# Kernel tuning notes

Measured on AMD Instinct MI355X. Metric: run time of the kernel, lower is better.

Reference implementation:

```python
import jax, jax.numpy as jnp
import numpy as np

EPS = 1e-5
NUM_HEADS = 16

def rmsnorm(x, w=None, eps=EPS):
    y = x * jax.lax.rsqrt(jnp.mean(x * x, axis=-1, keepdims=True) + eps)
    return y if w is None else y * w

def act_quant(x):
    # per-token 8-bit absmax activation quantization (BitNet b1.58)
    scale = 127.0 / jnp.clip(jnp.max(jnp.abs(x), axis=-1, keepdims=True), 1e-5, None)
    return jnp.clip(jnp.round(x * scale), -128, 127) / scale

def weight_quant(w):
    # ternary (1.58-bit) absmean weight quantization
    scale = 1.0 / jnp.clip(jnp.mean(jnp.abs(w)), 1e-5, None)
    return jnp.clip(jnp.round(w * scale), -1, 1) / scale

def bit_linear(x, w):
    # BitLinear: RMSNorm -> STE-quantized activation @ STE-quantized ternary weight
    xn = rmsnorm(x)
    xq = xn + jax.lax.stop_gradient(act_quant(xn) - xn)
    wq = w + jax.lax.stop_gradient(weight_quant(w) - w)
    return xq @ wq.T

def hgrn_recurrence(i, logf):
    # elementwise gated linear recurrence: h_t = exp(logf_t) * h_{t-1} + i_t
    def step(h, xs):
        ii, ff = xs
        h = jnp.exp(ff) * h + ii
        return h, h
    B, T, D = i.shape
    _, o = jax.lax.scan(step, jnp.zeros((B, D), i.dtype),
                        (jnp.swapaxes(i, 0, 1), jnp.swapaxes(logf, 0, 1)))
    return jnp.swapaxes(o, 0, 1)  # [B, T, D]

def hgrn_bit_attention(x, w_i, w_f, w_g, w_o, g_norm_w):
    i = bit_linear(x, w_i)
    f = bit_linear(x, w_f)
    logf = jax.nn.log_sigmoid(f)
    i = jax.nn.silu(i) * (1.0 - jax.nn.sigmoid(f))  # swiglu(i, 1 - sigmoid(f))
    o = hgrn_recurrence(i, logf)
    g = bit_linear(x, w_g)
    B, T, D = o.shape
    oh = rmsnorm(o.reshape(B, T, NUM_HEADS, D // NUM_HEADS), g_norm_w)  # per-head RMSNorm
    o = oh.reshape(B, T, D) * g * jax.nn.sigmoid(g)  # swish gate (FusedRMSNormSwishGate)
    return bit_linear(o, w_o)

def setup_inputs() -> dict:
    key = jax.random.key(0)
    B, S_S, S_C, D = 4, 4096, 512, 2048
    ks = jax.random.split(key, 16)
    mk = lambda k: jax.random.normal(k, (D, D), jnp.float32) * 0.02
    return {
        "hidden_states": jax.random.normal(ks[0], (B, S_S, D), jnp.float32),
        "encoder_hidden_states": jax.random.normal(ks[1], (B, S_C, D), jnp.float32),
        "w_q": mk(ks[2]), "w_k": mk(ks[3]), "w_v": mk(ks[4]), "w_out": mk(ks[5]),
        "w_add_q": mk(ks[6]), "w_add_k": mk(ks[7]), "w_add_v": mk(ks[8]), "w_add_out": mk(ks[9]),
        "w_i": mk(ks[10]), "w_f": mk(ks[11]), "w_g": mk(ks[12]), "w_o": mk(ks[13]),
        "g_norm_w": jnp.ones((D // NUM_HEADS,), jnp.float32),
    }

def reference(hidden_states, encoder_hidden_states, w_q, w_k, w_v, w_out,
              w_add_q, w_add_k, w_add_v, w_add_out, w_i, w_f, w_g, w_o, g_norm_w):
    q_s = bit_linear(hidden_states, w_q)
    k_s = bit_linear(hidden_states, w_k)          # computed as in original; unused by attn
    v_s = bit_linear(hidden_states, w_v)          # computed as in original; unused by attn
    q_c = bit_linear(encoder_hidden_states, w_add_q)
    k_c = bit_linear(encoder_hidden_states, w_add_k)
    v_c = bit_linear(encoder_hidden_states, w_add_v)
    q_joint = jnp.concatenate([q_c, q_s], axis=1)  # context first, then stream
    attn_out = hgrn_bit_attention(q_joint, w_i, w_f, w_g, w_o, g_norm_w)
    len_c = encoder_hidden_states.shape[1]
    out_c, out_s = attn_out[:, :len_c, :], attn_out[:, len_c:, :]
    return (bit_linear(out_s, w_out), bit_linear(out_c, w_add_out))
```

## Files before the change

kernel.cpp:

```cpp
#include <hip/hip_runtime.h>
#include <math.h>
#include <stdint.h>

#define D2 2048

typedef int v4i __attribute__((ext_vector_type(4)));
typedef int v16i __attribute__((ext_vector_type(16)));

struct Ptrs8 { const float* p[8]; };
struct RowMap { int seg, jump, off; };

enum { QW_Q = 0, QW_OUT = 1, QW_ADDQ = 2, QW_ADDOUT = 3, QW_I = 4, QW_F = 5, QW_G = 6, QW_O = 7 };

__device__ __forceinline__ int rmap(RowMap m, int r) {
  return (r / m.seg) * m.jump + (r % m.seg) + m.off;
}

__device__ __forceinline__ void gload16(const void* g, void* l) {
  __builtin_amdgcn_global_load_lds((__attribute__((address_space(1))) void*)g,
                                   (__attribute__((address_space(3))) void*)l, 16, 0, 0);
}

__device__ __forceinline__ float fsig(float x) {
  return __builtin_amdgcn_rcpf(1.0f + __expf(-x));
}

template <bool NT>
__device__ __forceinline__ void stf(float* p, float v) {
  if (NT) __builtin_nontemporal_store(v, p);
  else *p = v;
}

__device__ __forceinline__ void gswz(int nM, int& mb, int& nb) {
  int bid = blockIdx.x;
  int wg = (bid & 7) * (nM << 1) + (bid >> 3);
  mb = wg >> 4;
  nb = wg & 15;
}

__global__ __launch_bounds__(256) void k_wabs(Ptrs8 wsrc, double* part) {
  int m = blockIdx.y;
  const float4* w4 = (const float4*)(wsrc.p[m] + (size_t)blockIdx.x * 4096 + threadIdx.x * 16);
  double s = 0.0;
#pragma unroll
  for (int j = 0; j < 4; ++j) {
    float4 v = w4[j];
    s += (double)fabsf(v.x) + (double)fabsf(v.y) + (double)fabsf(v.z) + (double)fabsf(v.w);
  }
#pragma unroll
  for (int o = 32; o; o >>= 1) s += __shfl_down(s, o);
  __shared__ double red[4];
  if ((threadIdx.x & 63) == 0) red[threadIdx.x >> 6] = s;
  __syncthreads();
  if (threadIdx.x == 0) part[(size_t)m * 1024 + blockIdx.x] = red[0] + red[1] + red[2] + red[3];
}

__global__ __launch_bounds__(256) void k_wmean(const double* part, double* wqs, float* wmul) {
  int m = blockIdx.x, t = threadIdx.x;
  const double* p = part + (size_t)m * 1024;
  double s = p[t] + p[t + 256] + p[t + 512] + p[t + 768];
#pragma unroll
  for (int o = 32; o; o >>= 1) s += __shfl_down(s, o);
  __shared__ double red[4];
  if ((t & 63) == 0) red[t >> 6] = s;
  __syncthreads();
  if (t == 0) {
    double mean = (red[0] + red[1] + red[2] + red[3]) * (1.0 / 4194304.0);
    double cl = mean > 1e-5 ? mean : 1e-5;
    wqs[m] = 1.0 / cl;
    wmul[m] = (float)cl;
  }
}

__global__ __launch_bounds__(256) void k_wquant(Ptrs8 wsrc, const double* wqs, int8_t* wq) {
  int m = blockIdx.y;
  double qs = wqs[m];
  size_t base = (size_t)blockIdx.x * 4096 + threadIdx.x * 16;
  const float4* w4 = (const float4*)(wsrc.p[m] + base);
  union { int8_t b[16]; int4 v; } u;
#pragma unroll
  for (int j = 0; j < 4; ++j) {
    float4 v = w4[j];
    float f[4] = {v.x, v.y, v.z, v.w};
#pragma unroll
    for (int c = 0; c < 4; ++c) {
      int q = (int)rint((double)f[c] * qs);
      q = q > 1 ? 1 : (q < -1 ? -1 : q);
      u.b[j * 4 + c] = (int8_t)q;
    }
  }
  *(int4*)(wq + (size_t)m * 4194304 + base) = u.v;
}

__global__ __launch_bounds__(256) void k_actq(const float* __restrict__ x, int8_t* __restrict__ q,
                                              float* __restrict__ inv) {
  int row = blockIdx.x, t = threadIdx.x;
  const float4* xr = (const float4*)(x + (size_t)row * D2);
  float4 a = xr[t * 2], b = xr[t * 2 + 1];
  float v[8] = {a.x, a.y, a.z, a.w, b.x, b.y, b.z, b.w};
  float ss = 0.f, ma = 0.f;
#pragma unroll
  for (int j = 0; j < 8; ++j) { ss += v[j] * v[j]; ma = fmaxf(ma, fabsf(v[j])); }
#pragma unroll
  for (int o = 32; o; o >>= 1) { ss += __shfl_down(ss, o); ma = fmaxf(ma, __shfl_down(ma, o)); }
  __shared__ float rs[4], rm[4], bc[2];
  if ((t & 63) == 0) { rs[t >> 6] = ss; rm[t >> 6] = ma; }
  __syncthreads();
  if (t == 0) {
    float S = rs[0] + rs[1] + rs[2] + rs[3];
    float M = fmaxf(fmaxf(rm[0], rm[1]), fmaxf(rm[2], rm[3]));
    float r = 1.0f / sqrtf(S * (1.0f / 2048.0f) + 1e-5f);
    float mx = fmaxf(M * r, 1e-5f);
    bc[0] = r;
    bc[1] = 127.0f / mx;
    inv[row] = mx * (1.0f / 127.0f);
  }
  __syncthreads();
  float r = bc[0], s = bc[1];
  union { int8_t b8[8]; int2 p2; } u;
#pragma unroll
  for (int j = 0; j < 8; ++j) {
    float xn = v[j] * r;
    int qq = (int)rintf(xn * s);
    qq = qq > 127 ? 127 : (qq < -128 ? -128 : qq);
    u.b8[j] = (int8_t)qq;
  }
  ((int2*)(q + (size_t)row * D2))[t] = u.p2;
}

#define SYNC_PIPE(N)                                          \
  do {                                                        \
    __builtin_amdgcn_sched_barrier(0);                        \
    asm volatile("s_waitcnt vmcnt(" #N ")" ::: "memory");     \
    __builtin_amdgcn_sched_barrier(0);                        \
    __builtin_amdgcn_s_barrier();                             \
    __builtin_amdgcn_sched_barrier(0);                        \
  } while (0)

__device__ __forceinline__ void gemm_mainloop128(const int8_t* __restrict__ Aq,
                                                 const int8_t* __restrict__ Wq, int ga0, int ga1,
                                                 int n0, int t, int8_t* lds, v16i acc[2][2]) {
  const int wid = t >> 6, lane = t & 63;
  const int wr = wid >> 1, wc = wid & 1, am = lane & 31, g = lane >> 5;
  const int arow = t >> 2;
  const int achk = ((t & 3) ^ ((arow >> 1) & 3)) * 16;
  const int8_t* agp0 = Aq + (size_t)ga0 * 2048 + achk;
  const int8_t* agp1 = Aq + (size_t)ga1 * 2048 + achk;
  const int8_t* bgp0 = Wq + (size_t)(n0 + arow) * 2048 + achk;
  const int8_t* bgp1 = Wq + (size_t)(n0 + 64 + arow) * 2048 + achk;
  int8_t* A0 = lds;
  int8_t* B0 = lds + 8192;
  int8_t* A1 = lds + 16384;
  int8_t* B1 = lds + 24576;
  int8_t* A2 = lds + 32768;
  int8_t* B2 = lds + 40960;

#define STAGE128(Ab, Bb)                              \
  do {                                                \
    gload16(agp0, (Ab) + wid * 1024);                 \
    gload16(agp1, (Ab) + 4096 + wid * 1024);          \
    gload16(bgp0, (Bb) + wid * 1024);                 \
    gload16(bgp1, (Bb) + 4096 + wid * 1024);          \
    agp0 += 64; agp1 += 64; bgp0 += 64; bgp1 += 64;   \
  } while (0)

#define COMPUTE128(Ab, Bb)                                                                  \
  do {                                                                                      \
    _Pragma("unroll") for (int kk = 0; kk < 2; ++kk) {                                      \
      v4i af[2], bf[2];                                                                     \
      _Pragma("unroll") for (int mi = 0; mi < 2; ++mi) {                                    \
        int r = wr * 64 + mi * 32 + am;                                                     \
        int slot = ((kk << 1) | g) ^ ((r >> 1) & 3);                                        \
        af[mi] = *(const v4i*)((Ab) + r * 64 + slot * 16);                                  \
        int rb = wc * 64 + mi * 32 + am;                                                    \
        int slotb = ((kk << 1) | g) ^ ((rb >> 1) & 3);                                      \
        bf[mi] = *(const v4i*)((Bb) + rb * 64 + slotb * 16);                                \
      }                                                                                     \
      _Pragma("unroll") for (int mi = 0; mi < 2; ++mi)                                      \
        _Pragma("unroll") for (int ni = 0; ni < 2; ++ni)                                    \
          acc[mi][ni] =                                                                     \
              __builtin_amdgcn_mfma_i32_32x32x32_i8(af[mi], bf[ni], acc[mi][ni], 0, 0, 0);  \
    }                                                                                       \
  } while (0)

  STAGE128(A0, B0);
  STAGE128(A1, B1);
  STAGE128(A2, B2);
  SYNC_PIPE(8);
#pragma unroll 1
  for (int tt = 0; tt < 30; tt += 3) {
    COMPUTE128(A0, B0);
    SYNC_PIPE(4);
    if (tt + 3 < 32) STAGE128(A0, B0);
    COMPUTE128(A1, B1);
    SYNC_PIPE(4);
    if (tt + 4 < 32) STAGE128(A1, B1);
    COMPUTE128(A2, B2);
    SYNC_PIPE(4);
    if (tt + 5 < 32) STAGE128(A2, B2);
  }
  COMPUTE128(A0, B0);
  SYNC_PIPE(0);
  COMPUTE128(A1, B1);
#undef STAGE128
#undef COMPUTE128
}

template <bool NT>
__device__ __forceinline__ void gemm_body(const int8_t* Aq, const float* ainv, const int8_t* Wq,
                                          const float* wmul, int widx, float* C, RowMap inm,
                                          RowMap outm, int m0, int n0, int t, int8_t* lds) {
  int lane = t & 63, wid = t >> 6;
  int wr = wid >> 1, wc = wid & 1;
  int am = lane & 31, g = lane >> 5;
  int ga0 = rmap(inm, m0 + (t >> 2));
  int ga1 = rmap(inm, m0 + 64 + (t >> 2));

  v16i acc[2][2] = {};
  gemm_mainloop128(Aq, Wq, ga0, ga1, n0, t, lds, acc);

  float wm = wmul[widx];
#pragma unroll
  for (int mi = 0; mi < 2; ++mi) {
#pragma unroll
    for (int q = 0; q < 16; ++q) {
      int rin = wr * 64 + mi * 32 + (q & 3) + ((q >> 2) * 8) + g * 4;
      int ra = rmap(inm, m0 + rin);
      int rc = rmap(outm, m0 + rin);
      float s = ainv[ra] * wm;
#pragma unroll
      for (int ni = 0; ni < 2; ++ni) {
        stf<NT>(&C[(size_t)rc * 2048 + n0 + wc * 64 + ni * 32 + am], (float)acc[mi][ni][q] * s);
      }
    }
  }
}

template <bool NT>
__global__ __launch_bounds__(256) void k_gemm(const int8_t* __restrict__ Aq,
                                              const float* __restrict__ ainv,
                                              const int8_t* __restrict__ Wq,
                                              const float* __restrict__ wmul, int widx,
                                              float* __restrict__ C, RowMap inm, RowMap outm,
                                              int nM) {
  __shared__ __align__(16) int8_t lds[49152];
  int mb, nb;
  gswz(nM, mb, nb);
  gemm_body<NT>(Aq, ainv, Wq, wmul, widx, C, inm, outm, mb * 128, nb * 128, threadIdx.x, lds);
}

template <bool NT>
__global__ __launch_bounds__(256) void k_gemm2(const int8_t* __restrict__ Aq,
                                               const float* __restrict__ ainv,
                                               const int8_t* __restrict__ W0, int w0idx,
                                               RowMap inm0, RowMap outm0, float* __restrict__ C0,
                                               int nM0,
                                               const int8_t* __restrict__ W1, int w1idx,
                                               RowMap inm1, RowMap outm1, float* __restrict__ C1,
                                               int nM1, const float* __restrict__ wmul) {
  __shared__ __align__(16) int8_t lds[49152];
  int mb, nb;
  gswz(nM0 + nM1, mb, nb);
  if (mb < nM0) {
    gemm_body<NT>(Aq, ainv, W0, wmul, w0idx, C0, inm0, outm0, mb * 128, nb * 128, threadIdx.x,
                  lds);
  } else {
    gemm_body<NT>(Aq, ainv, W1, wmul, w1idx, C1, inm1, outm1, (mb - nM0) * 128, nb * 128,
                  threadIdx.x, lds);
  }
}

__global__ __launch_bounds__(256) void k_gemm_if(const int8_t* __restrict__ Aq,
                                                 const float* __restrict__ ainv,
                                                 const int8_t* __restrict__ Wi,
                                                 const int8_t* __restrict__ Wf,
                                                 const float* __restrict__ wmul,
                                                 float* __restrict__ IG, float* __restrict__ AD,
                                                 int nM) {
  __shared__ __align__(16) int8_t lds[73728];
  int mb, nb;
  gswz(nM, mb, nb);
  int m0 = mb * 128, n0 = nb * 128;
  int t = threadIdx.x;
  const int wid = t >> 6, lane = t & 63;
  const int wr = wid >> 1, wc = wid & 1, am = lane & 31, g = lane >> 5;
  const int arow = t >> 2;
  const int achk = ((t & 3) ^ ((arow >> 1) & 3)) * 16;
  const int8_t* agp0 = Aq + (size_t)(m0 + arow) * 2048 + achk;
  const int8_t* agp1 = Aq + (size_t)(m0 + 64 + arow) * 2048 + achk;
  const int8_t* bip0 = Wi + (size_t)(n0 + arow) * 2048 + achk;
  const int8_t* bip1 = Wi + (size_t)(n0 + 64 + arow) * 2048 + achk;
  const int8_t* bfp0 = Wf + (size_t)(n0 + arow) * 2048 + achk;
  const int8_t* bfp1 = Wf + (size_t)(n0 + 64 + arow) * 2048 + achk;

  v16i acci[2][2] = {};
  v16i accf[2][2] = {};

#define STAGE_IF(B)                                                                   \
  do {                                                                                \
    gload16(agp0, lds + (B) + wid * 1024);                                            \
    gload16(agp1, lds + (B) + 4096 + wid * 1024);                                     \
    gload16(bip0, lds + (B) + 8192 + wid * 1024);                                     \
    gload16(bip1, lds + (B) + 12288 + wid * 1024);                                    \
    gload16(bfp0, lds + (B) + 16384 + wid * 1024);                                    \
    gload16(bfp1, lds + (B) + 20480 + wid * 1024);                                    \
    agp0 += 64; agp1 += 64; bip0 += 64; bip1 += 64; bfp0 += 64; bfp1 += 64;           \
  } while (0)

#define COMPUTE_IF(B)                                                                       \
  do {                                                                                      \
    _Pragma("unroll") for (int kk = 0; kk < 2; ++kk) {                                      \
      v4i af[2], bfi[2], bff[2];                                                            \
      _Pragma("unroll") for (int mi = 0; mi < 2; ++mi) {                                    \
        int r = wr * 64 + mi * 32 + am;                                                     \
        int slot = ((kk << 1) | g) ^ ((r >> 1) & 3);                                        \
        af[mi] = *(const v4i*)(lds + (B) + r * 64 + slot * 16);                             \
      }                                                                                     \
      _Pragma("unroll") for (int ni = 0; ni < 2; ++ni) {                                    \
        int rb = wc * 64 + ni * 32 + am;                                                    \
        int slotb = ((kk << 1) | g) ^ ((rb >> 1) & 3);                                      \
        bfi[ni] = *(const v4i*)(lds + (B) + 8192 + rb * 64 + slotb * 16);                   \
        bff[ni] = *(const v4i*)(lds + (B) + 16384 + rb * 64 + slotb * 16);                  \
      }                                                                                     \
      _Pragma("unroll") for (int mi = 0; mi < 2; ++mi)                                      \
        _Pragma("unroll") for (int ni = 0; ni < 2; ++ni) {                                  \
          acci[mi][ni] =                                                                    \
              __builtin_amdgcn_mfma_i32_32x32x32_i8(af[mi], bfi[ni], acci[mi][ni], 0, 0, 0);\
          accf[mi][ni] =                                                                    \
              __builtin_amdgcn_mfma_i32_32x32x32_i8(af[mi], bff[ni], accf[mi][ni], 0, 0, 0);\
        }                                                                                   \
    }                                                                                       \
  } while (0)

  STAGE_IF(0);
  STAGE_IF(24576);
  STAGE_IF(49152);
  SYNC_PIPE(12);
#pragma unroll 1
  for (int tt = 0; tt < 30; tt += 3) {
    COMPUTE_IF(0);
    SYNC_PIPE(6);
    if (tt + 3 < 32) STAGE_IF(0);
    COMPUTE_IF(24576);
    SYNC_PIPE(6);
    if (tt + 4 < 32) STAGE_IF(24576);
    COMPUTE_IF(49152);
    SYNC_PIPE(6);
    if (tt + 5 < 32) STAGE_IF(49152);
  }
  COMPUTE_IF(0);
  SYNC_PIPE(0);
  COMPUTE_IF(24576);
#undef STAGE_IF
#undef COMPUTE_IF

  float wmi = wmul[QW_I], wmf = wmul[QW_F];
#pragma unroll
  for (int mi = 0; mi < 2; ++mi) {
#pragma unroll
    for (int q = 0; q < 16; ++q) {
      int rin = m0 + wr * 64 + mi * 32 + (q & 3) + ((q >> 2) * 8) + g * 4;
      float si = ainv[rin] * wmi;
      float sf = ainv[rin] * wmf;
#pragma unroll
      for (int ni = 0; ni < 2; ++ni) {
        size_t idx = (size_t)rin * 2048 + n0 + wc * 64 + ni * 32 + am;
        float iv = (float)acci[mi][ni][q] * si;
        float fv = (float)accf[mi][ni][q] * sf;
        float a = fsig(fv);
        float s2 = iv * fsig(iv);
        __builtin_nontemporal_store(s2 * (1.0f - a), &IG[idx]);
        __builtin_nontemporal_store(a, &AD[idx]);
      }
    }
  }
}

__global__ __launch_bounds__(256) void k_rec1(const float* __restrict__ ig,
                                              const float* __restrict__ ad,
                                              float* __restrict__ chA, float* __restrict__ chH) {
  int tid = blockIdx.x * 256 + threadIdx.x;
  int chain = tid & 8191;
  int c = tid >> 13;
  int b = chain >> 11, d = chain & 2047;
  size_t base = ((size_t)b * 4608 + (size_t)c * 72) * 2048 + d;
  float h = 0.f, P = 1.f;
  for (int s = 0; s < 72; ++s) {
    float av = ad[base];
    float iv = __builtin_nontemporal_load(ig + base);
    h = av * h + iv;
    P *= av;
    base += 2048;
  }
  chA[(size_t)c * 8192 + chain] = P;
  chH[(size_t)c * 8192 + chain] = h;
}

__global__ __launch_bounds__(256) void k_rec2(const float* __restrict__ chA,
                                              const float* __restrict__ chH,
                                              float* __restrict__ chC) {
  int chain = blockIdx.x * 256 + threadIdx.x;
  float carry = 0.f;
  for (int c = 0; c < 64; ++c) {
    chC[(size_t)c * 8192 + chain] = carry;
    carry = chA[(size_t)c * 8192 + chain] * carry + chH[(size_t)c * 8192 + chain];
  }
}

__global__ __launch_bounds__(256) void k_rec3(float* __restrict__ io, const float* __restrict__ ad,
                                              const float* __restrict__ chC) {
  int tid = blockIdx.x * 256 + threadIdx.x;
  int chain = tid & 8191;
  int c = tid >> 13;
  int b = chain >> 11, d = chain & 2047;
  size_t base = ((size_t)b * 4608 + (size_t)c * 72) * 2048 + d;
  float h = chC[(size_t)c * 8192 + chain];
  for (int s = 0; s < 72; ++s) {
    float av = ad[base];
    float iv = io[base];
    h = av * h + iv;
    io[base] = h;
    base += 2048;
  }
}

__global__ __launch_bounds__(256) void k_hnq(const float* __restrict__ o,
                                             const float* __restrict__ g,
                                             const float* __restrict__ gnw,
                                             int8_t* __restrict__ q, float* __restrict__ inv) {
  int row = blockIdx.x, t = threadIdx.x;
  size_t base = (size_t)row * D2 + (size_t)t * 8;
  float4 a = *(const float4*)(o + base);
  float4 b = *(const float4*)(o + base + 4);
  float v[8] = {a.x, a.y, a.z, a.w, b.x, b.y, b.z, b.w};
  float ss = 0.f;
#pragma unroll
  for (int j = 0; j < 8; ++j) ss += v[j] * v[j];
  ss += __shfl_xor(ss, 1);
  ss += __shfl_xor(ss, 2);
  ss += __shfl_xor(ss, 4);
  ss += __shfl_xor(ss, 8);
  float r = 1.0f / sqrtf(ss * (1.0f / 128.0f) + 1e-5f);
  float4 ga = *(const float4*)(g + base);
  float4 gb = *(const float4*)(g + base + 4);
  float gv[8] = {ga.x, ga.y, ga.z, ga.w, gb.x, gb.y, gb.z, gb.w};
  int j0 = (t & 15) * 8;
  float o2[8];
#pragma unroll
  for (int j = 0; j < 8; ++j) {
    float gg = gv[j];
    o2[j] = v[j] * r * gnw[j0 + j] * gg * fsig(gg);
  }
  float ss2 = 0.f, ma = 0.f;
#pragma unroll
  for (int j = 0; j < 8; ++j) { ss2 += o2[j] * o2[j]; ma = fmaxf(ma, fabsf(o2[j])); }
#pragma unroll
  for (int off = 32; off; off >>= 1) {
    ss2 += __shfl_down(ss2, off);
    ma = fmaxf(ma, __shfl_down(ma, off));
  }
  __shared__ float rs[4], rm[4], bc[2];
  if ((t & 63) == 0) { rs[t >> 6] = ss2; rm[t >> 6] = ma; }
  __syncthreads();
  if (t == 0) {
    float S = rs[0] + rs[1] + rs[2] + rs[3];
    float M = fmaxf(fmaxf(rm[0], rm[1]), fmaxf(rm[2], rm[3]));
    float rr = 1.0f / sqrtf(S * (1.0f / 2048.0f) + 1e-5f);
    float mx = fmaxf(M * rr, 1e-5f);
    bc[0] = rr;
    bc[1] = 127.0f / mx;
    inv[row] = mx * (1.0f / 127.0f);
  }
  __syncthreads();
  float rr = bc[0], s = bc[1];
  union { int8_t b8[8]; int2 p2; } u;
#pragma unroll
  for (int j = 0; j < 8; ++j) {
    float xn = o2[j] * rr;
    int qq = (int)rintf(xn * s);
    qq = qq > 127 ? 127 : (qq < -128 ? -128 : qq);
    u.b8[j] = (int8_t)qq;
  }
  ((int2*)(q + (size_t)row * D2))[t] = u.p2;
}

extern "C" void kernel_launch(void* const* d_in, const int* in_sizes, int n_in,
                              void* d_out, int out_size, void* d_ws, size_t ws_size,
                              hipStream_t stream) {
  const float* hid = (const float*)d_in[0];
  const float* enc = (const float*)d_in[1];
  const float* gnw = (const float*)d_in[14];
  Ptrs8 wp;
  wp.p[QW_Q] = (const float*)d_in[2];
  wp.p[QW_OUT] = (const float*)d_in[5];
  wp.p[QW_ADDQ] = (const float*)d_in[6];
  wp.p[QW_ADDOUT] = (const float*)d_in[9];
  wp.p[QW_I] = (const float*)d_in[10];
  wp.p[QW_F] = (const float*)d_in[11];
  wp.p[QW_G] = (const float*)d_in[12];
  wp.p[QW_O] = (const float*)d_in[13];
  float* out = (float*)d_out;

  char* ws = (char*)d_ws;
  float* bufA = (float*)ws;
  float* bufB = bufA + 37748736;
  int8_t* actq = (int8_t*)(bufB + 37748736);
  int8_t* wq = actq + 37748736;
  float* ainv = (float*)(wq + 33554432);
  double* wpart = (double*)(ainv + 18432);
  double* wqs = wpart + 8192;
  float* wmul = (float*)(wqs + 8);
  float* chA = wmul + 8;
  float* chH = chA + 524288;
  float* chC = chH + 524288;
  if (ws_size < 379723872ULL) return;

  RowMap idm{0x40000000, 0, 0};
  RowMap encoff{0x40000000, 0, 16384};
  RowMap seqm{4096, 4608, 512};
  RowMap encm{512, 4608, 0};

  k_wabs<<<dim3(1024, 8), 256, 0, stream>>>(wp, wpart);
  k_wmean<<<8, 256, 0, stream>>>(wpart, wqs, wmul);
  k_wquant<<<dim3(1024, 8), 256, 0, stream>>>(wp, wqs, wq);
  k_actq<<<16384, 256, 0, stream>>>(hid, actq, ainv);
  k_actq<<<2048, 256, 0, stream>>>(enc, actq + (size_t)16384 * 2048, ainv + 16384);
  k_gemm2<false><<<(128 + 16) * 16, 256, 0, stream>>>(
      actq, ainv, wq + (size_t)QW_Q * 4194304, QW_Q, idm, seqm, bufA, 128,
      wq + (size_t)QW_ADDQ * 4194304, QW_ADDQ, encoff, encm, bufA, 16, wmul);
  k_actq<<<18432, 256, 0, stream>>>(bufA, actq, ainv);
  k_gemm_if<<<144 * 16, 256, 0, stream>>>(actq, ainv, wq + (size_t)QW_I * 4194304,
                                          wq + (size_t)QW_F * 4194304, wmul, bufA, bufB, 144);
  k_gemm<true><<<144 * 16, 256, 0, stream>>>(actq, ainv, wq + (size_t)QW_G * 4194304, wmul,
                                             QW_G, out, idm, idm, 144);
  k_rec1<<<2048, 256, 0, stream>>>(bufA, bufB, chA, chH);
  k_rec2<<<32, 256, 0, stream>>>(chA, chH, chC);
  k_rec3<<<2048, 256, 0, stream>>>(bufA, bufB, chC);
  k_hnq<<<18432, 256, 0, stream>>>(bufA, out, gnw, actq, ainv);
  k_gemm<false><<<144 * 16, 256, 0, stream>>>(actq, ainv, wq + (size_t)QW_O * 4194304, wmul,
                                              QW_O, bufB, idm, idm, 144);
  k_actq<<<18432, 256, 0, stream>>>(bufB, actq, ainv);
  k_gemm2<true><<<(128 + 16) * 16, 256, 0, stream>>>(
      actq, ainv, wq + (size_t)QW_OUT * 4194304, QW_OUT, seqm, idm, out, 128,
      wq + (size_t)QW_ADDOUT * 4194304, QW_ADDOUT, encm, idm, out + (size_t)33554432, 16, wmul);
}
```

Before: 965.1 us.

## Widen single-GEMM tiles to 128x256 and extend LDS swizzle

The generic int8 GEMM kernels move from 128x128 to 128x256 output tiles. Each warp now computes a 2x4 grid of 32x32 MFMA blocks, which raises arithmetic intensity per LDS A-tile load and halves the grid size. The group swizzle is changed to match the 8 column blocks. LDS use grows to 72KB with the triple-buffer pipeline kept, and the LDS XOR swizzle gains a second row-bit term to cut bank conflicts. The cost is more accumulator registers and fewer blocks in flight, which may lower occupancy.

New measurement: 965.0 us. About the same (-0.0%).

```diff
diff --git a/kernel.cpp b/kernel.cpp
--- a/kernel.cpp
+++ b/kernel.cpp
@@ -31,11 +31,19 @@
   else *p = v;
 }
 
-__device__ __forceinline__ void gswz(int nM, int& mb, int& nb) {
+__device__ __forceinline__ int swz(int r) { return ((r >> 1) & 3) ^ ((r >> 3) & 3); }
+
+__device__ __forceinline__ void gswz16(int nM, int& mb, int& nb) {
   int bid = blockIdx.x;
   int wg = (bid & 7) * (nM << 1) + (bid >> 3);
   mb = wg >> 4;
   nb = wg & 15;
+}
+__device__ __forceinline__ void gswz8(int nM, int& mb, int& nb) {
+  int bid = blockIdx.x;
+  int wg = (bid & 7) * nM + (bid >> 3);
+  mb = wg >> 3;
+  nb = wg & 7;
 }
 
 __global__ __launch_bounds__(256) void k_wabs(Ptrs8 wsrc, double* part) {
@@ -137,73 +145,74 @@
     __builtin_amdgcn_sched_barrier(0);                        \
   } while (0)
 
-__device__ __forceinline__ void gemm_mainloop128(const int8_t* __restrict__ Aq,
-                                                 const int8_t* __restrict__ Wq, int ga0, int ga1,
-                                                 int n0, int t, int8_t* lds, v16i acc[2][2]) {
+__device__ __forceinline__ void gemm_mainloop(const int8_t* __restrict__ Aq,
+                                              const int8_t* __restrict__ Wq, int ga0, int ga1,
+                                              int n0, int t, int8_t* lds, v16i acc[2][4]) {
   const int wid = t >> 6, lane = t & 63;
   const int wr = wid >> 1, wc = wid & 1, am = lane & 31, g = lane >> 5;
   const int arow = t >> 2;
-  const int achk = ((t & 3) ^ ((arow >> 1) & 3)) * 16;
+  const int achk = ((t & 3) ^ swz(arow)) * 16;
   const int8_t* agp0 = Aq + (size_t)ga0 * 2048 + achk;
   const int8_t* agp1 = Aq + (size_t)ga1 * 2048 + achk;
   const int8_t* bgp0 = Wq + (size_t)(n0 + arow) * 2048 + achk;
   const int8_t* bgp1 = Wq + (size_t)(n0 + 64 + arow) * 2048 + achk;
-  int8_t* A0 = lds;
-  int8_t* B0 = lds + 8192;
-  int8_t* A1 = lds + 16384;
-  int8_t* B1 = lds + 24576;
-  int8_t* A2 = lds + 32768;
-  int8_t* B2 = lds + 40960;
-
-#define STAGE128(Ab, Bb)                              \
-  do {                                                \
-    gload16(agp0, (Ab) + wid * 1024);                 \
-    gload16(agp1, (Ab) + 4096 + wid * 1024);          \
-    gload16(bgp0, (Bb) + wid * 1024);                 \
-    gload16(bgp1, (Bb) + 4096 + wid * 1024);          \
-    agp0 += 64; agp1 += 64; bgp0 += 64; bgp1 += 64;   \
+  const int8_t* bgp2 = Wq + (size_t)(n0 + 128 + arow) * 2048 + achk;
+  const int8_t* bgp3 = Wq + (size_t)(n0 + 192 + arow) * 2048 + achk;
+
+#define STAGEW(B)                                                \
+  do {                                                           \
+    gload16(agp0, lds + (B) + wid * 1024);                       \
+    gload16(agp1, lds + (B) + 4096 + wid * 1024);                \
+    gload16(bgp0, lds + (B) + 8192 + wid * 1024);                \
+    gload16(bgp1, lds + (B) + 12288 + wid * 1024);               \
+    gload16(bgp2, lds + (B) + 16384 + wid * 1024);               \
+    gload16(bgp3, lds + (B) + 20480 + wid * 1024);               \
+    agp0 += 64; agp1 += 64;                                      \
+    bgp0 += 64; bgp1 += 64; bgp2 += 64; bgp3 += 64;              \
   } while (0)
 
-#define COMPUTE128(Ab, Bb)                                                                  \
+#define COMPUTEW(B)                                                                         \
   do {                                                                                      \
     _Pragma("unroll") for (int kk = 0; kk < 2; ++kk) {                                      \
-      v4i af[2], bf[2];                                                                     \
+      v4i af[2], bf[4];                                                                     \
       _Pragma("unroll") for (int mi = 0; mi < 2; ++mi) {                                    \
         int r = wr * 64 + mi * 32 + am;                                                     \
-        int slot = ((kk << 1) | g) ^ ((r >> 1) & 3);                                        \
-        af[mi] = *(const v4i*)((Ab) + r * 64 + slot * 16);                                  \
-        int rb = wc * 64 + mi * 32 + am;                                                    \
-        int slotb = ((kk << 1) | g) ^ ((rb >> 1) & 3);                                      \
-        bf[mi] = *(const v4i*)((Bb) + rb * 64 + slotb * 16);                                \
+        int slot = ((kk << 1) | g) ^ swz(r);                                                \
+        af[mi] = *(const v4i*)(lds + (B) + r * 64 + slot * 16);                             \
+      }                                                                                     \
+      _Pragma("unroll") for (int ni = 0; ni < 4; ++ni) {                                    \
+        int rb = wc * 128 + ni * 32 + am;                                                   \
+        int slotb = ((kk << 1) | g) ^ swz(rb);                                              \
+        bf[ni] = *(const v4i*)(lds + (B) + 8192 + rb * 64 + slotb * 16);                    \
       }                                                                                     \
       _Pragma("unroll") for (int mi = 0; mi < 2; ++mi)                                      \
-        _Pragma("unroll") for (int ni = 0; ni < 2; ++ni)                                    \
+        _Pragma("unroll") for (int ni = 0; ni < 4; ++ni)                                    \
           acc[mi][ni] =                                                                     \
               __builtin_amdgcn_mfma_i32_32x32x32_i8(af[mi], bf[ni], acc[mi][ni], 0, 0, 0);  \
     }                                                                                       \
   } while (0)
 
-  STAGE128(A0, B0);
-  STAGE128(A1, B1);
-  STAGE128(A2, B2);
-  SYNC_PIPE(8);
+  STAGEW(0);
+  STAGEW(24576);
+  STAGEW(49152);
+  SYNC_PIPE(12);
 #pragma unroll 1
   for (int tt = 0; tt < 30; tt += 3) {
-    COMPUTE128(A0, B0);
-    SYNC_PIPE(4);
-    if (tt + 3 < 32) STAGE128(A0, B0);
-    COMPUTE128(A1, B1);
-    SYNC_PIPE(4);
-    if (tt + 4 < 32) STAGE128(A1, B1);
-    COMPUTE128(A2, B2);
-    SYNC_PIPE(4);
-    if (tt + 5 < 32) STAGE128(A2, B2);
-  }
-  COMPUTE128(A0, B0);
+    COMPUTEW(0);
+    SYNC_PIPE(6);
+    if (tt + 3 < 32) STAGEW(0);
+    COMPUTEW(24576);
+    SYNC_PIPE(6);
+    if (tt + 4 < 32) STAGEW(24576);
+    COMPUTEW(49152);
+    SYNC_PIPE(6);
+    if (tt + 5 < 32) STAGEW(49152);
+  }
+  COMPUTEW(0);
   SYNC_PIPE(0);
-  COMPUTE128(A1, B1);
-#undef STAGE128
-#undef COMPUTE128
+  COMPUTEW(24576);
+#undef STAGEW
+#undef COMPUTEW
 }
 
 template <bool NT>
@@ -216,8 +225,8 @@
   int ga0 = rmap(inm, m0 + (t >> 2));
   int ga1 = rmap(inm, m0 + 64 + (t >> 2));
 
-  v16i acc[2][2] = {};
-  gemm_mainloop128(Aq, Wq, ga0, ga1, n0, t, lds, acc);
+  v16i acc[2][4] = {};
+  gemm_mainloop(Aq, Wq, ga0, ga1, n0, t, lds, acc);
 
   float wm = wmul[widx];
 #pragma unroll
@@ -229,8 +238,8 @@
       int rc = rmap(outm, m0 + rin);
       float s = ainv[ra] * wm;
 #pragma unroll
-      for (int ni = 0; ni < 2; ++ni) {
-        stf<NT>(&C[(size_t)rc * 2048 + n0 + wc * 64 + ni * 32 + am], (float)acc[mi][ni][q] * s);
+      for (int ni = 0; ni < 4; ++ni) {
+        stf<NT>(&C[(size_t)rc * 2048 + n0 + wc * 128 + ni * 32 + am], (float)acc[mi][ni][q] * s);
       }
     }
   }
@@ -243,10 +252,10 @@
                                               const float* __restrict__ wmul, int widx,
                                               float* __restrict__ C, RowMap inm, RowMap outm,
                                               int nM) {
-  __shared__ __align__(16) int8_t lds[49152];
+  __shared__ __align__(16) int8_t lds[73728];
   int mb, nb;
-  gswz(nM, mb, nb);
-  gemm_body<NT>(Aq, ainv, Wq, wmul, widx, C, inm, outm, mb * 128, nb * 128, threadIdx.x, lds);
+  gswz8(nM, mb, nb);
+  gemm_body<NT>(Aq, ainv, Wq, wmul, widx, C, inm, outm, mb * 128, nb * 256, threadIdx.x, lds);
 }
 
 template <bool NT>
@@ -258,14 +267,14 @@
                                                const int8_t* __restrict__ W1, int w1idx,
                                                RowMap inm1, RowMap outm1, float* __restrict__ C1,
                                                int nM1, const float* __restrict__ wmul) {
-  __shared__ __align__(16) int8_t lds[49152];
+  __shared__ __align__(16) int8_t lds[73728];
   int mb, nb;
-  gswz(nM0 + nM1, mb, nb);
+  gswz8(nM0 + nM1, mb, nb);
   if (mb < nM0) {
-    gemm_body<NT>(Aq, ainv, W0, wmul, w0idx, C0, inm0, outm0, mb * 128, nb * 128, threadIdx.x,
+    gemm_body<NT>(Aq, ainv, W0, wmul, w0idx, C0, inm0, outm0, mb * 128, nb * 256, threadIdx.x,
                   lds);
   } else {
-    gemm_body<NT>(Aq, ainv, W1, wmul, w1idx, C1, inm1, outm1, (mb - nM0) * 128, nb * 128,
+    gemm_body<NT>(Aq, ainv, W1, wmul, w1idx, C1, inm1, outm1, (mb - nM0) * 128, nb * 256,
                   threadIdx.x, lds);
   }
 }
@@ -279,13 +288,13 @@
                                                  int nM) {
   __shared__ __align__(16) int8_t lds[73728];
   int mb, nb;
-  gswz(nM, mb, nb);
+  gswz16(nM, mb, nb);
   int m0 = mb * 128, n0 = nb * 128;
   int t = threadIdx.x;
   const int wid = t >> 6, lane = t & 63;
   const int wr = wid >> 1, wc = wid & 1, am = lane & 31, g = lane >> 5;
   const int arow = t >> 2;
-  const int achk = ((t & 3) ^ ((arow >> 1) & 3)) * 16;
+  const int achk = ((t & 3) ^ swz(arow)) * 16;
   const int8_t* agp0 = Aq + (size_t)(m0 + arow) * 2048 + achk;
   const int8_t* agp1 = Aq + (size_t)(m0 + 64 + arow) * 2048 + achk;
   const int8_t* bip0 = Wi + (size_t)(n0 + arow) * 2048 + achk;
@@ -313,12 +322,12 @@
       v4i af[2], bfi[2], bff[2];                                                            \
       _Pragma("unroll") for (int mi = 0; mi < 2; ++mi) {                                    \
         int r = wr * 64 + mi * 32 + am;                                                     \
-        int slot = ((kk << 1) | g) ^ ((r >> 1) & 3);                                        \
+        int slot = ((kk << 1) | g) ^ swz(r);                                                \
         af[mi] = *(const v4i*)(lds + (B) + r * 64 + slot * 16);                             \
       }                                                                                     \
       _Pragma("unroll") for (int ni = 0; ni < 2; ++ni) {                                    \
         int rb = wc * 64 + ni * 32 + am;                                                    \
-        int slotb = ((kk << 1) | g) ^ ((rb >> 1) & 3);                                      \
+        int slotb = ((kk << 1) | g) ^ swz(rb);                                              \
         bfi[ni] = *(const v4i*)(lds + (B) + 8192 + rb * 64 + slotb * 16);                   \
         bff[ni] = *(const v4i*)(lds + (B) + 16384 + rb * 64 + slotb * 16);                  \
       }                                                                                     \
@@ -525,22 +534,22 @@
   k_wquant<<<dim3(1024, 8), 256, 0, stream>>>(wp, wqs, wq);
   k_actq<<<16384, 256, 0, stream>>>(hid, actq, ainv);
   k_actq<<<2048, 256, 0, stream>>>(enc, actq + (size_t)16384 * 2048, ainv + 16384);
-  k_gemm2<false><<<(128 + 16) * 16, 256, 0, stream>>>(
+  k_gemm2<false><<<(128 + 16) * 8, 256, 0, stream>>>(
       actq, ainv, wq + (size_t)QW_Q * 4194304, QW_Q, idm, seqm, bufA, 128,
       wq + (size_t)QW_ADDQ * 4194304, QW_ADDQ, encoff, encm, bufA, 16, wmul);
   k_actq<<<18432, 256, 0, stream>>>(bufA, actq, ainv);
   k_gemm_if<<<144 * 16, 256, 0, stream>>>(actq, ainv, wq + (size_t)QW_I * 4194304,
                                           wq + (size_t)QW_F * 4194304, wmul, bufA, bufB, 144);
-  k_gemm<true><<<144 * 16, 256, 0, stream>>>(actq, ainv, wq + (size_t)QW_G * 4194304, wmul,
-                                             QW_G, out, idm, idm, 144);
+  k_gemm<true><<<144 * 8, 256, 0, stream>>>(actq, ainv, wq + (size_t)QW_G * 4194304, wmul,
+                                            QW_G, out, idm, idm, 144);
   k_rec1<<<2048, 256, 0, stream>>>(bufA, bufB, chA, chH);
   k_rec2<<<32, 256, 0, stream>>>(chA, chH, chC);
   k_rec3<<<2048, 256, 0, stream>>>(bufA, bufB, chC);
   k_hnq<<<18432, 256, 0, stream>>>(bufA, out, gnw, actq, ainv);
-  k_gemm<false><<<144 * 16, 256, 0, stream>>>(actq, ainv, wq + (size_t)QW_O * 4194304, wmul,
-                                              QW_O, bufB, idm, idm, 144);
+  k_gemm<false><<<144 * 8, 256, 0, stream>>>(actq, ainv, wq + (size_t)QW_O * 4194304, wmul,
+                                             QW_O, bufB, idm, idm, 144);
   k_actq<<<18432, 256, 0, stream>>>(bufB, actq, ainv);
-  k_gemm2<true><<<(128 + 16) * 16, 256, 0, stream>>>(
+  k_gemm2<true><<<(128 + 16) * 8, 256, 0, stream>>>(
       actq, ainv, wq + (size_t)QW_OUT * 4194304, QW_OUT, seqm, idm, out, 128,
       wq + (size_t)QW_ADDOUT * 4194304, QW_ADDOUT, encm, idm, out + (size_t)33554432, 16, wmul);
 }
```
